# Kernel optimization log

Measured on AMD Instinct MI355X. Metric: run time of the kernel, lower is better.

Reference implementation:

```python
import jax, jax.numpy as jnp
import numpy as np
import math

B, T, D = 2, 2048, 1024
H = 16
DH = D // H
DFF = 4096
EPS = 1e-5


def setup_inputs() -> dict:
    key = jax.random.key(0)
    ks = jax.random.split(key, 10)
    x = jax.random.normal(ks[0], (B, T, D), dtype=jnp.float32)
    # bool mask, True above diagonal => masked (matches masked_fill semantics)
    causal_mask = jnp.triu(jnp.ones((T, T), dtype=bool), k=1)
    s = 0.02
    return {
        "x": x,
        "causal_mask": causal_mask,
        "gamma1": jnp.ones((D,), jnp.float32),
        "beta1": jnp.zeros((D,), jnp.float32),
        "wq": jax.random.normal(ks[1], (D, D), jnp.float32) * s,
        "wk": jax.random.normal(ks[2], (D, D), jnp.float32) * s,
        "wv": jax.random.normal(ks[3], (D, D), jnp.float32) * s,
        "wo": jax.random.normal(ks[4], (D, D), jnp.float32) * s,
        "gamma2": jnp.ones((D,), jnp.float32),
        "beta2": jnp.zeros((D,), jnp.float32),
        "w1": jax.random.normal(ks[5], (D, DFF), jnp.float32) * s,
        "b1": jnp.zeros((DFF,), jnp.float32),
        "w2": jax.random.normal(ks[6], (DFF, D), jnp.float32) * s,
        "b2": jnp.zeros((D,), jnp.float32),
    }


def _layer_norm(x, gamma, beta):
    mean = jnp.mean(x, axis=-1, keepdims=True)
    var = jnp.mean((x - mean) ** 2, axis=-1, keepdims=True)
    xhat = (x - mean) / jnp.sqrt(var + EPS)
    return gamma * xhat + beta


def _split_heads(x):
    b, t, d = x.shape
    return x.reshape(b, t, H, DH).transpose(0, 2, 1, 3)  # (B,H,T,Dh)


def reference(x, causal_mask, gamma1, beta1, wq, wk, wv, wo,
              gamma2, beta2, w1, b1, w2, b2):
    # --- attention sublayer (pre-LN) ---
    h = _layer_norm(x, gamma1, beta1)
    q = _split_heads(h @ wq)
    k = _split_heads(h @ wk)
    v = _split_heads(h @ wv)
    scores = jnp.einsum('bhqd,bhkd->bhqk', q, k) / math.sqrt(DH)  # (B,H,T,T)
    scores = jnp.where(causal_mask[None, None, :, :], -jnp.inf, scores)
    attn = jax.nn.softmax(scores, axis=-1)
    out = jnp.einsum('bhqk,bhkd->bhqd', attn, v)
    out = out.transpose(0, 2, 1, 3).reshape(x.shape)  # merge heads
    attn_out = out @ wo
    x = x + attn_out
    # --- FFN sublayer (pre-LN) ---
    h = _layer_norm(x, gamma2, beta2)
    ffn = jax.nn.gelu(h @ w1 + b1, approximate=False) @ w2 + b2
    return x + ffn
```

## Files before the change

### kernel.cpp

```cpp
#include <hip/hip_runtime.h>
#include <hip/hip_bf16.h>
#include <math.h>

#define B_   2
#define T_   2048
#define D_   1024
#define H_   16
#define DH_  64
#define DFF_ 4096
#define NTOK (B_*T_)

typedef __attribute__((ext_vector_type(8))) short short8;
typedef __attribute__((ext_vector_type(4))) float f32x4;

static __device__ __forceinline__ short f2bf(float f) {
    union { __hip_bfloat16 h; short s; } u;
    u.h = __float2bfloat16(f);
    return u.s;
}

static __device__ __forceinline__ f32x4 mfma16(short8 a, short8 b, f32x4 c) {
    return __builtin_amdgcn_mfma_f32_16x16x32_bf16(a, b, c, 0, 0, 0);
}

static __device__ __forceinline__ void gload16(const void* g, void* l) {
    __builtin_amdgcn_global_load_lds(
        (__attribute__((address_space(1))) void*)g,
        (__attribute__((address_space(3))) void*)l, 16, 0, 0);
}

static __device__ __forceinline__ short8 lds_read_sw(const short* base, int row, int kbyte) {
    const int off = (row << 7) + (kbyte ^ ((row & 7) << 4));
    return *reinterpret_cast<const short8*>(reinterpret_cast<const char*>(base) + off);
}

__global__ __launch_bounds__(256) void transpose_cast(
    const float* __restrict__ src, short* __restrict__ dst, int K, int N, float scale)
{
    __shared__ short tile[32][33];
    const int k0 = blockIdx.y * 32, n0 = blockIdx.x * 32;
    const int tx = threadIdx.x, ty = threadIdx.y;
    #pragma unroll
    for (int j = 0; j < 4; ++j) {
        int k = ty + j * 8;
        tile[k][tx] = f2bf(src[(size_t)(k0 + k) * N + n0 + tx] * scale);
    }
    __syncthreads();
    #pragma unroll
    for (int j = 0; j < 4; ++j) {
        int n = ty + j * 8;
        dst[(size_t)(n0 + n) * K + k0 + tx] = tile[tx][n];
    }
}

__global__ __launch_bounds__(256) void ln_kernel(
    const float* __restrict__ in, const float* __restrict__ gamma,
    const float* __restrict__ beta, short* __restrict__ out)
{
    const int row = blockIdx.x;
    const int t = threadIdx.x;
    const float4 v = *reinterpret_cast<const float4*>(in + (size_t)row * D_ + t * 4);
    float s  = v.x + v.y + v.z + v.w;
    float sq = v.x*v.x + v.y*v.y + v.z*v.z + v.w*v.w;
    #pragma unroll
    for (int off = 32; off >= 1; off >>= 1) {
        s  += __shfl_xor(s, off);
        sq += __shfl_xor(sq, off);
    }
    __shared__ float ps[4], pq[4];
    if ((t & 63) == 0) { ps[t >> 6] = s; pq[t >> 6] = sq; }
    __syncthreads();
    s  = ps[0] + ps[1] + ps[2] + ps[3];
    sq = pq[0] + pq[1] + pq[2] + pq[3];
    const float mean = s * (1.0f / D_);
    float var = sq * (1.0f / D_) - mean * mean;
    var = fmaxf(var, 0.0f);
    const float rstd = rsqrtf(var + 1e-5f);
    const float4 g = *reinterpret_cast<const float4*>(gamma + t * 4);
    const float4 b = *reinterpret_cast<const float4*>(beta  + t * 4);
    short4 o;
    o.x = f2bf(g.x * ((v.x - mean) * rstd) + b.x);
    o.y = f2bf(g.y * ((v.y - mean) * rstd) + b.y);
    o.z = f2bf(g.z * ((v.z - mean) * rstd) + b.z);
    o.w = f2bf(g.w * ((v.w - mean) * rstd) + b.w);
    *reinterpret_cast<short4*>(out + (size_t)row * D_ + t * 4) = o;
}

template<int BM, int BN, int EPI>
__global__ __launch_bounds__(512) void gemm_kernel(
    const short* __restrict__ A, const short* __restrict__ Bt,
    void* __restrict__ Cout, const float* __restrict__ resid,
    const float* __restrict__ bias, short* __restrict__ vaux,
    int M, int N, int K, int nbx)
{
    constexpr int MB = BM / 4 / 16;
    constexpr int NB = BN / 2 / 16;
    constexpr int JA = BM / 64;
    constexpr int JB = BN / 64;
    __shared__ short As[2][BM * 64];
    __shared__ short Bs[2][BN * 64];
    const int t = threadIdx.x;
    const int wid = t >> 6, lane = t & 63;
    const int lr = lane & 15, lk = lane >> 4;
    const int cpx = (int)gridDim.x >> 3;
    const int bid = (int)blockIdx.x;
    const int swz = (bid & 7) * cpx + (bid >> 3);
    const int m0 = (swz / nbx) * BM, n0 = (swz % nbx) * BN;
    const int wrow = (wid >> 1) * (BM / 4);
    const int wcol = (wid & 1) * (BN / 2);

    const char* aSrc[JA];
    const char* bSrc[JB];
    #pragma unroll
    for (int j = 0; j < JA; ++j) {
        const int off = j * 8192 + t * 16;
        const int r   = off >> 7;
        const int cb  = (off & 127) ^ ((r & 7) << 4);
        aSrc[j] = (const char*)(A + (size_t)(m0 + r) * K) + cb;
    }
    #pragma unroll
    for (int j = 0; j < JB; ++j) {
        const int off = j * 8192 + t * 16;
        const int r   = off >> 7;
        const int cb  = (off & 127) ^ ((r & 7) << 4);
        bSrc[j] = (const char*)(Bt + (size_t)(n0 + r) * K) + cb;
    }

    f32x4 acc[MB][NB];
    #pragma unroll
    for (int m = 0; m < MB; ++m)
        #pragma unroll
        for (int n = 0; n < NB; ++n) acc[m][n] = (f32x4){0.f, 0.f, 0.f, 0.f};

    const int NT = K >> 6;

    #pragma unroll
    for (int j = 0; j < JA; ++j)
        gload16(aSrc[j], (char*)As[0] + j * 8192 + wid * 1024);
    #pragma unroll
    for (int j = 0; j < JB; ++j)
        gload16(bSrc[j], (char*)Bs[0] + j * 8192 + wid * 1024);
    __syncthreads();

    int cur = 0;
    for (int kt = 0; kt < NT; ++kt) {
        if (kt + 1 < NT) {
            const int kb = (kt + 1) << 7;
            #pragma unroll
            for (int j = 0; j < JA; ++j)
                gload16(aSrc[j] + kb, (char*)As[cur ^ 1] + j * 8192 + wid * 1024);
            #pragma unroll
            for (int j = 0; j < JB; ++j)
                gload16(bSrc[j] + kb, (char*)Bs[cur ^ 1] + j * 8192 + wid * 1024);
        }
        #pragma unroll
        for (int kk = 0; kk < 64; kk += 32) {
            short8 af[MB], bf[NB];
            #pragma unroll
            for (int m = 0; m < MB; ++m)
                af[m] = lds_read_sw(As[cur], wrow + m * 16 + lr, (kk + lk * 8) * 2);
            #pragma unroll
            for (int n = 0; n < NB; ++n)
                bf[n] = lds_read_sw(Bs[cur], wcol + n * 16 + lr, (kk + lk * 8) * 2);
            #pragma unroll
            for (int m = 0; m < MB; ++m)
                #pragma unroll
                for (int n = 0; n < NB; ++n)
                    acc[m][n] = mfma16(af[m], bf[n], acc[m][n]);
        }
        __syncthreads();
        cur ^= 1;
    }

    #pragma unroll
    for (int m = 0; m < MB; ++m) {
        #pragma unroll
        for (int n = 0; n < NB; ++n) {
            #pragma unroll
            for (int r = 0; r < 4; ++r) {
                const int gr = m0 + wrow + m * 16 + lk * 4 + r;
                const int gc = n0 + wcol + n * 16 + lr;
                const size_t idx = (size_t)gr * N + gc;
                const float v = acc[m][n][r];
                if constexpr (EPI == 0) {
                    ((short*)Cout)[idx] = f2bf(v);
                } else if constexpr (EPI == 1) {
                    ((float*)Cout)[idx] = resid[idx] + v;
                } else if constexpr (EPI == 2) {
                    const float tt = v + bias[gc];
                    const float ge = 0.5f * tt * (1.0f + erff(tt * 0.70710678118654752f));
                    ((short*)Cout)[idx] = f2bf(ge);
                } else if constexpr (EPI == 3) {
                    ((float*)Cout)[idx] = resid[idx] + v + bias[gc];
                } else {
                    if (gc < 2048) {
                        ((short*)Cout)[idx] = f2bf(v);
                    } else {
                        const int hh = (gc - 2048) >> 6, dh = (gc - 2048) & 63;
                        const int bb = gr >> 11, tl = gr & 2047;
                        vaux[((size_t)((bb << 4) + hh) * 64 + dh) * 2048 + tl] = f2bf(v);
                    }
                }
            }
        }
    }
}

static __device__ __forceinline__ void attn_tile(
    const short* Kcur, const short* Vcur, char* pw,
    short8 qf0, short8 qf1, int q0, int kvb, bool diag,
    int lr, int lk, f32x4 (&o)[4], float (&mr)[4], float (&ls)[4])
{
    f32x4 s[4];
    #pragma unroll
    for (int n = 0; n < 4; ++n) s[n] = (f32x4){0.f, 0.f, 0.f, 0.f};
    #pragma unroll
    for (int n = 0; n < 4; ++n) {
        s[n] = mfma16(qf0, lds_read_sw(Kcur, n * 16 + lr, (lk * 8) * 2), s[n]);
        s[n] = mfma16(qf1, lds_read_sw(Kcur, n * 16 + lr, (32 + lk * 8) * 2), s[n]);
    }
    #pragma unroll
    for (int r = 0; r < 4; ++r) {
        const int qg = q0 + lk * 4 + r;
        float v0 = s[0][r], v1 = s[1][r], v2 = s[2][r], v3 = s[3][r];
        if (diag) {
            if (kvb +      lr > qg) v0 = -INFINITY;
            if (kvb + 16 + lr > qg) v1 = -INFINITY;
            if (kvb + 32 + lr > qg) v2 = -INFINITY;
            if (kvb + 48 + lr > qg) v3 = -INFINITY;
        }
        const float mxl = fmaxf(fmaxf(v0, v1), fmaxf(v2, v3));
        if (!__all(mxl <= mr[r] + 8.0f)) {
            float mx = mxl;
            mx = fmaxf(mx, __shfl_xor(mx, 1));
            mx = fmaxf(mx, __shfl_xor(mx, 2));
            mx = fmaxf(mx, __shfl_xor(mx, 4));
            mx = fmaxf(mx, __shfl_xor(mx, 8));
            const float mnew = fmaxf(mr[r], mx);
            const float alpha = __builtin_amdgcn_exp2f(mr[r] - mnew);
            o[0][r] *= alpha; o[1][r] *= alpha; o[2][r] *= alpha; o[3][r] *= alpha;
            ls[r] *= alpha;
            mr[r] = mnew;
        }
        const float p0 = __builtin_amdgcn_exp2f(v0 - mr[r]);
        const float p1 = __builtin_amdgcn_exp2f(v1 - mr[r]);
        const float p2 = __builtin_amdgcn_exp2f(v2 - mr[r]);
        const float p3 = __builtin_amdgcn_exp2f(v3 - mr[r]);
        ls[r] += p0 + p1 + p2 + p3;
        const int prow = lk * 4 + r;
        const int sw = (prow & 7) << 4;
        char* prb = pw + prow * 128;
        *(short*)(prb + (((     lr * 2)) ^ sw)) = f2bf(p0);
        *(short*)(prb + ((32 + lr * 2) ^ sw)) = f2bf(p1);
        *(short*)(prb + ((64 + lr * 2) ^ sw)) = f2bf(p2);
        *(short*)(prb + ((96 + lr * 2) ^ sw)) = f2bf(p3);
    }
    asm volatile("s_waitcnt lgkmcnt(0)" ::: "memory");
    #pragma unroll
    for (int kk = 0; kk < 2; ++kk) {
        const short8 pf = *reinterpret_cast<const short8*>(
            pw + lr * 128 + ((kk * 64 + lk * 16) ^ ((lr & 7) << 4)));
        #pragma unroll
        for (int n = 0; n < 4; ++n)
            o[n] = mfma16(pf, lds_read_sw((const short*)Vcur, n * 16 + lr, (kk * 32 + lk * 8) * 2), o[n]);
    }
}

__global__ __launch_bounds__(256) void attn_kernel(
    const short* __restrict__ qkv, const short* __restrict__ vT,
    short* __restrict__ attn)
{
    __shared__ short Ks[2][4096];
    __shared__ short Vs[2][4096];
    __shared__ short Ps[2][4][1024];
    const int xx = blockIdx.x;
    const int bh = blockIdx.y;
    const int qA = xx, qB = 31 - xx;
    const int b = bh >> 4, h = bh & 15;
    const int t = threadIdx.x;
    const int wid = t >> 6, lane = t & 63;
    const int lr = lane & 15, lk = lane >> 4;
    const int q0A = qA * 64 + wid * 16;
    const int q0B = qB * 64 + wid * 16;

    const short* qrowA = qkv + (size_t)(b * T_ + q0A + lr) * 3072 + h * 64;
    const short8 qfA0 = *reinterpret_cast<const short8*>(qrowA + lk * 8);
    const short8 qfA1 = *reinterpret_cast<const short8*>(qrowA + 32 + lk * 8);
    const short* qrowB = qkv + (size_t)(b * T_ + q0B + lr) * 3072 + h * 64;
    const short8 qfB0 = *reinterpret_cast<const short8*>(qrowB + lk * 8);
    const short8 qfB1 = *reinterpret_cast<const short8*>(qrowB + 32 + lk * 8);
    const short* kbase = qkv + (size_t)b * T_ * 3072 + 1024 + h * 64;
    const short* vbase = vT + (size_t)bh * 64 * T_;

    f32x4 oA[4], oB[4];
    float mrA[4], lsA[4], mrB[4], lsB[4];
    #pragma unroll
    for (int n = 0; n < 4; ++n) {
        oA[n] = (f32x4){0.f, 0.f, 0.f, 0.f};
        oB[n] = (f32x4){0.f, 0.f, 0.f, 0.f};
    }
    #pragma unroll
    for (int r = 0; r < 4; ++r) {
        mrA[r] = -INFINITY; lsA[r] = 0.f;
        mrB[r] = -INFINITY; lsB[r] = 0.f;
    }

    const int nkt = qB + 1;

    #pragma unroll
    for (int j = 0; j < 2; ++j) {
        const int off = j * 4096 + t * 16;
        const int r   = off >> 7;
        const int cb  = (off & 127) ^ ((r & 7) << 4);
        gload16(kbase + (size_t)r * 3072 + (cb >> 1), (char*)Ks[0] + j * 4096 + wid * 1024);
        gload16(vbase + (size_t)r * T_   + (cb >> 1), (char*)Vs[0] + j * 4096 + wid * 1024);
    }
    __syncthreads();

    int cur = 0;
    for (int kt = 0; kt < nkt; ++kt) {
        const int kvb = kt * 64;
        if (kt + 1 < nkt) {
            const int nb = kvb + 64;
            #pragma unroll
            for (int j = 0; j < 2; ++j) {
                const int off = j * 4096 + t * 16;
                const int r   = off >> 7;
                const int cb  = (off & 127) ^ ((r & 7) << 4);
                gload16(kbase + (size_t)(nb + r) * 3072 + (cb >> 1),
                        (char*)Ks[cur ^ 1] + j * 4096 + wid * 1024);
                gload16(vbase + (size_t)r * T_ + nb + (cb >> 1),
                        (char*)Vs[cur ^ 1] + j * 4096 + wid * 1024);
            }
        }

        attn_tile(Ks[cur], Vs[cur], (char*)&Ps[1][wid][0],
                  qfB0, qfB1, q0B, kvb, kt == qB, lr, lk, oB, mrB, lsB);
        if (kt <= qA)
            attn_tile(Ks[cur], Vs[cur], (char*)&Ps[0][wid][0],
                      qfA0, qfA1, q0A, kvb, kt == qA, lr, lk, oA, mrA, lsA);

        __syncthreads();
        cur ^= 1;
    }

    #pragma unroll
    for (int r = 0; r < 4; ++r) {
        float lA = lsA[r], lB = lsB[r];
        lA += __shfl_xor(lA, 1); lB += __shfl_xor(lB, 1);
        lA += __shfl_xor(lA, 2); lB += __shfl_xor(lB, 2);
        lA += __shfl_xor(lA, 4); lB += __shfl_xor(lB, 4);
        lA += __shfl_xor(lA, 8); lB += __shfl_xor(lB, 8);
        const float invA = 1.0f / lA, invB = 1.0f / lB;
        short* opA = attn + (size_t)(b * T_ + q0A + lk * 4 + r) * D_ + h * 64;
        short* opB = attn + (size_t)(b * T_ + q0B + lk * 4 + r) * D_ + h * 64;
        #pragma unroll
        for (int n = 0; n < 4; ++n) {
            opA[n * 16 + lr] = f2bf(oA[n][r] * invA);
            opB[n * 16 + lr] = f2bf(oB[n][r] * invB);
        }
    }
}

extern "C" void kernel_launch(void* const* d_in, const int* in_sizes, int n_in,
                              void* d_out, int out_size, void* d_ws, size_t ws_size,
                              hipStream_t stream)
{
    (void)in_sizes; (void)n_in; (void)out_size; (void)ws_size;
    const float* x      = (const float*)d_in[0];
    const float* gamma1 = (const float*)d_in[2];
    const float* beta1  = (const float*)d_in[3];
    const float* wq     = (const float*)d_in[4];
    const float* wk     = (const float*)d_in[5];
    const float* wv     = (const float*)d_in[6];
    const float* wo     = (const float*)d_in[7];
    const float* gamma2 = (const float*)d_in[8];
    const float* beta2  = (const float*)d_in[9];
    const float* w1     = (const float*)d_in[10];
    const float* b1     = (const float*)d_in[11];
    const float* w2     = (const float*)d_in[12];
    const float* b2     = (const float*)d_in[13];
    float* out = (float*)d_out;

    char* ws = (char*)d_ws;
    size_t off = 0;
    short* wqkvT = (short*)(ws + off); off += (size_t)3072 * 1024 * 2;
    short* woT   = (short*)(ws + off); off += (size_t)1024 * 1024 * 2;
    short* w1T   = (short*)(ws + off); off += (size_t)4096 * 1024 * 2;
    short* w2T   = (short*)(ws + off); off += (size_t)1024 * 4096 * 2;
    short* h1    = (short*)(ws + off); off += (size_t)NTOK * 1024 * 2;
    short* h2    = (short*)(ws + off); off += (size_t)NTOK * 1024 * 2;
    float* y     = (float*)(ws + off); off += (size_t)NTOK * 1024 * 4;
    short* attnb = (short*)(ws + off); off += (size_t)NTOK * 1024 * 2;
    short* qkv   = (short*)(ws + off); off += (size_t)NTOK * 3072 * 2;
    short* vT    = (short*)(ws + off); off += (size_t)B_ * H_ * DH_ * T_ * 2;
    short* g     = qkv;

    const dim3 tb(32, 8);
    transpose_cast<<<dim3(32, 32),  tb, 0, stream>>>(wq, wqkvT,               1024, 1024, 0.18033688011112042f);
    transpose_cast<<<dim3(32, 32),  tb, 0, stream>>>(wk, wqkvT + 1024 * 1024, 1024, 1024, 1.0f);
    transpose_cast<<<dim3(32, 32),  tb, 0, stream>>>(wv, wqkvT + 2048 * 1024, 1024, 1024, 1.0f);
    transpose_cast<<<dim3(32, 32),  tb, 0, stream>>>(wo, woT,                 1024, 1024, 1.0f);
    transpose_cast<<<dim3(128, 32), tb, 0, stream>>>(w1, w1T, 1024, 4096, 1.0f);
    transpose_cast<<<dim3(32, 128), tb, 0, stream>>>(w2, w2T, 4096, 1024, 1.0f);

    ln_kernel<<<NTOK, 256, 0, stream>>>(x, gamma1, beta1, h1);

    gemm_kernel<128, 128, 4><<<768, 512, 0, stream>>>(
        h1, wqkvT, qkv, nullptr, nullptr, vT, NTOK, 3072, 1024, 24);

    attn_kernel<<<dim3(16, 32), 256, 0, stream>>>(qkv, vT, attnb);

    gemm_kernel<128, 64, 1><<<512, 512, 0, stream>>>(
        attnb, woT, y, x, nullptr, nullptr, NTOK, 1024, 1024, 16);

    ln_kernel<<<NTOK, 256, 0, stream>>>(y, gamma2, beta2, h2);

    gemm_kernel<128, 128, 2><<<1024, 512, 0, stream>>>(
        h2, w1T, g, nullptr, b1, nullptr, NTOK, 4096, 1024, 32);

    gemm_kernel<128, 64, 3><<<512, 512, 0, stream>>>(
        g, w2T, out, y, b2, nullptr, NTOK, 1024, 4096, 16);
}
```

Baseline: 261.9 us.

## Triple-buffer GEMM shared-memory tiles with vmcnt-based waits

Changes the GEMM main loop from double to triple buffering of A/B tiles in LDS, prefetching two K-tiles ahead. Replaces the full __syncthreads with a partial s_waitcnt vmcnt plus s_barrier so the newest tile's loads can remain in flight during compute. This hides more global-to-LDS latency but raises LDS usage by half, which may reduce occupancy.

New measurement: 300.2 us. 1.15x slower.

```diff
diff --git a/kernel.cpp b/kernel.cpp
--- a/kernel.cpp
+++ b/kernel.cpp
@@ -97,8 +97,9 @@
     constexpr int NB = BN / 2 / 16;
     constexpr int JA = BM / 64;
     constexpr int JB = BN / 64;
-    __shared__ short As[2][BM * 64];
-    __shared__ short Bs[2][BN * 64];
+    constexpr int J  = JA + JB;
+    __shared__ short As[3][BM * 64];
+    __shared__ short Bs[3][BN * 64];
     const int t = threadIdx.x;
     const int wid = t >> 6, lane = t & 63;
     const int lr = lane & 15, lk = lane >> 4;
@@ -134,43 +135,45 @@
 
     const int NT = K >> 6;
 
-    #pragma unroll
-    for (int j = 0; j < JA; ++j)
-        gload16(aSrc[j], (char*)As[0] + j * 8192 + wid * 1024);
-    #pragma unroll
-    for (int j = 0; j < JB; ++j)
-        gload16(bSrc[j], (char*)Bs[0] + j * 8192 + wid * 1024);
-    __syncthreads();
-
-    int cur = 0;
-    for (int kt = 0; kt < NT; ++kt) {
-        if (kt + 1 < NT) {
-            const int kb = (kt + 1) << 7;
-            #pragma unroll
-            for (int j = 0; j < JA; ++j)
-                gload16(aSrc[j] + kb, (char*)As[cur ^ 1] + j * 8192 + wid * 1024);
-            #pragma unroll
-            for (int j = 0; j < JB; ++j)
-                gload16(bSrc[j] + kb, (char*)Bs[cur ^ 1] + j * 8192 + wid * 1024);
-        }
+    auto stage = [&](int bufsel, int ktile) {
+        const int kb = ktile << 7;
+        #pragma unroll
+        for (int j = 0; j < JA; ++j)
+            gload16(aSrc[j] + kb, (char*)As[bufsel] + j * 8192 + wid * 1024);
+        #pragma unroll
+        for (int j = 0; j < JB; ++j)
+            gload16(bSrc[j] + kb, (char*)Bs[bufsel] + j * 8192 + wid * 1024);
+    };
+    auto compute = [&](int bufsel) {
         #pragma unroll
         for (int kk = 0; kk < 64; kk += 32) {
             short8 af[MB], bf[NB];
             #pragma unroll
             for (int m = 0; m < MB; ++m)
-                af[m] = lds_read_sw(As[cur], wrow + m * 16 + lr, (kk + lk * 8) * 2);
+                af[m] = lds_read_sw(As[bufsel], wrow + m * 16 + lr, (kk + lk * 8) * 2);
             #pragma unroll
             for (int n = 0; n < NB; ++n)
-                bf[n] = lds_read_sw(Bs[cur], wcol + n * 16 + lr, (kk + lk * 8) * 2);
+                bf[n] = lds_read_sw(Bs[bufsel], wcol + n * 16 + lr, (kk + lk * 8) * 2);
             #pragma unroll
             for (int m = 0; m < MB; ++m)
                 #pragma unroll
                 for (int n = 0; n < NB; ++n)
                     acc[m][n] = mfma16(af[m], bf[n], acc[m][n]);
         }
-        __syncthreads();
-        cur ^= 1;
-    }
+    };
+
+    stage(0, 0);
+    stage(1, 1);
+
+    for (int kt = 0; kt < NT - 1; ++kt) {
+        asm volatile("s_waitcnt vmcnt(%0)" :: "n"(J) : "memory");
+        __builtin_amdgcn_s_barrier();
+        if (kt + 2 < NT) stage((kt + 2) % 3, kt + 2);
+        compute(kt % 3);
+    }
+    asm volatile("s_waitcnt vmcnt(0)" ::: "memory");
+    __builtin_amdgcn_s_barrier();
+    compute((NT - 1) % 3);
 
     #pragma unroll
     for (int m = 0; m < MB; ++m) {
```
